# Kernel optimization log

Measured on AMD Instinct MI355X. Metric: run time of the kernel, lower is better.

Reference implementation:

```python
import jax, jax.numpy as jnp
import numpy as np
from jax import lax

WIN = 15      # sliding window size
BINS = 64     # luminance histogram bins
ALPHA = 0.9   # local vs global histogram mix
LAM1 = 0.5    # a-channel (material) removal weight
LAM2 = 0.5    # b-channel (material) removal weight
EPS = 1e-6


def _box_sum(x, win):
    return lax.reduce_window(x, 0.0, lax.add, (1, win, win, 1), (1, 1, 1, 1), 'SAME')


def setup_inputs() -> dict:
    key = jax.random.key(0)
    u = jax.random.uniform(key, (4, 3, 512, 512), dtype=jnp.float32)
    L = u[:, 0] * 100.0                 # L in [0,100]
    a = u[:, 1] * 255.0 - 128.0         # a in [-128,127]
    b = u[:, 2] * 255.0 - 128.0         # b in [-128,127]
    return {"batch_lab_raw": jnp.stack([L, a, b], axis=1)}


def reference(batch_lab_raw):
    # Normalize channels
    Ln = jnp.clip(batch_lab_raw[:, 0] / 100.0, 0.0, 1.0)      # (B,H,W)
    an = (batch_lab_raw[:, 1] + 128.0) / 255.0                # (B,H,W)
    bn = (batch_lab_raw[:, 2] + 128.0) / 255.0                # (B,H,W)

    # --- windowed luminance histogram anomaly ---
    idx = jnp.clip((Ln * BINS).astype(jnp.int32), 0, BINS - 1)            # (B,H,W)
    onehot = jax.nn.one_hot(idx, BINS, dtype=Ln.dtype)                    # (B,H,W,K)
    cnt = _box_sum(onehot, WIN)                                           # (B,H,W,K)
    n = _box_sum(jnp.ones(Ln.shape + (1,), Ln.dtype), WIN)                # (B,H,W,1) valid-pixel count
    # probability of own bin within local window
    p_loc = jnp.take_along_axis(cnt / n, idx[..., None], axis=-1)[..., 0]  # (B,H,W)
    # global per-image histogram probability of own bin
    p_glob_bins = jnp.mean(onehot, axis=(1, 2))                            # (B,K)
    p_glob = jnp.einsum('bhwk,bk->bhw', onehot, p_glob_bins)              # (B,H,W)

    S = -jnp.log(ALPHA * p_loc + (1.0 - ALPHA) * p_glob + EPS)            # surprise
    S_min = jnp.min(S, axis=(1, 2), keepdims=True)
    S_max = jnp.max(S, axis=(1, 2), keepdims=True)
    L_anom_norm = (S - S_min) / (S_max - S_min + EPS)                     # (B,H,W)

    # --- de-materialized illumination: remove local chroma (material) variation ---
    mu_a = _box_sum(an[..., None], WIN)[..., 0] / n[..., 0]
    mu_b = _box_sum(bn[..., None], WIN)[..., 0] / n[..., 0]
    L_perp = jnp.clip(Ln - LAM1 * (an - mu_a) - LAM2 * (bn - mu_b), 0.0, 1.0)

    return (L_perp[:, None], L_anom_norm[:, None])  # each (B,1,H,W)
```

## Files before the change

### kernel.cpp

```cpp
#include <hip/hip_runtime.h>

#define Hh 512
#define Ww 512
#define NPIX (Hh*Ww)
#define BATCH 4


__global__ __launch_bounds__(256) void k_hist(const float* __restrict__ in,
                                              unsigned* __restrict__ hp) {
    __shared__ unsigned lh[64];
    const int tid = threadIdx.x;
    if (tid < 64) lh[tid] = 0u;
    __syncthreads();
    const int img = blockIdx.x >> 6, sub = blockIdx.x & 63;
    const float4* Lp = (const float4*)(in + (size_t)img * 3 * NPIX) + sub * 1024;
    #pragma unroll
    for (int t = 0; t < 4; ++t) {
        float4 v = Lp[t*256 + tid];
        float f[4] = {v.x, v.y, v.z, v.w};
        #pragma unroll
        for (int j = 0; j < 4; ++j) {
            float ln = fminf(fmaxf(f[j] / 100.0f, 0.0f), 1.0f);
            int idx = min((int)(ln * 64.0f), 63);
            atomicAdd(&lh[idx], 1u);
        }
    }
    __syncthreads();
    if (tid < 64) hp[(img*64 + sub)*64 + tid] = lh[tid];
}

__global__ __launch_bounds__(256, 8) void k_main(const float* __restrict__ in,
        const unsigned* __restrict__ hp, float* __restrict__ bmin,
        float* __restrict__ bmax, float* __restrict__ out)
{
    __shared__ unsigned s_pk[46*12];
    __shared__ float s_c[46*36];
    __shared__ float s_cc[32*33];
    __shared__ float s_lnc[32*16];
    __shared__ float lhf[64];
    __shared__ float red[8];

    const int tx = threadIdx.x, ty = threadIdx.y;
    const int tid = ty*16 + tx;
    const int bx = blockIdx.x * 16, by = blockIdx.y * 32;
    const int img = blockIdx.z;
    const float* Lp = in + (size_t)img * 3 * NPIX;

    if (tid < 64) {
        unsigned sum = 0;
        const unsigned* p = hp + img*4096 + tid;
        #pragma unroll 8
        for (int q = 0; q < 64; ++q) sum += p[q*64];
        lhf[tid] = (float)sum * (1.0f/262144.0f);
    }

    const int s = tx + 1;
    const int j0 = s >> 2;
    const unsigned m20 = 0x7FFFu << (s & 3);
    unsigned wm[5];
    #pragma unroll
    for (int i = 0; i < 5; ++i) {
        unsigned n = (m20 >> (4*i)) & 0xFu;
        wm[i] = (n&1u)*0x80u | (n&2u)*0x4000u | (n&4u)*0x200000u | (n&8u)*0x10000000u;
    }

    for (int l = tid; l < 368; l += 256) {
        const int r = l >> 3, c4 = l & 7;
        const int gy = by - 7 + r;
        const int gx0 = bx - 8 + c4*4;
        unsigned pk = 0x7F7F7F7Fu;
        float4 cv = {0.f, 0.f, 0.f, 0.f};
        if (gy >= 0 && gy < Hh && gx0 >= 0 && gx0 < Ww) {
            const int g = gy*Ww + gx0;
            const float4 Lv = *(const float4*)(Lp + g);
            const float4 Av = *(const float4*)(Lp + NPIX + g);
            const float4 Bv = *(const float4*)(Lp + 2*NPIX + g);
            const float l0 = fminf(fmaxf(Lv.x / 100.0f, 0.0f), 1.0f);
            const float l1 = fminf(fmaxf(Lv.y / 100.0f, 0.0f), 1.0f);
            const float l2 = fminf(fmaxf(Lv.z / 100.0f, 0.0f), 1.0f);
            const float l3 = fminf(fmaxf(Lv.w / 100.0f, 0.0f), 1.0f);
            const int b0 = min((int)(l0*64.0f), 63), b1 = min((int)(l1*64.0f), 63);
            const int b2 = min((int)(l2*64.0f), 63), b3 = min((int)(l3*64.0f), 63);
            pk = (unsigned)b0 | ((unsigned)b1<<8) | ((unsigned)b2<<16) | ((unsigned)b3<<24);
            const float k255 = 1.0f/255.0f;
            cv.x = (Av.x+128.0f)*k255 + (Bv.x+128.0f)*k255;
            cv.y = (Av.y+128.0f)*k255 + (Bv.y+128.0f)*k255;
            cv.z = (Av.z+128.0f)*k255 + (Bv.z+128.0f)*k255;
            cv.w = (Av.w+128.0f)*k255 + (Bv.w+128.0f)*k255;
            if (r >= 7 && r < 39 && c4 >= 2 && c4 <= 5) {
                float4 lv4 = {l0, l1, l2, l3};
                *(float4*)&s_lnc[(r-7)*16 + 4*(c4-2)] = lv4;
            }
        }
        s_pk[r*12 + c4] = pk;
        *(float4*)&s_c[r*36 + c4*4] = cv;
    }
    for (int l = tid; l < 184; l += 256) s_pk[(l>>2)*12 + 8 + (l&3)] = 0u;
    __syncthreads();

    for (int l = tid; l < 512; l += 256) {
        const int q = l >> 5, c = l & 31;
        float mid = 0.f;
        #pragma unroll
        for (int k = 1; k < 15; ++k) mid += s_c[(2*q+k)*36 + c];
        s_cc[(2*q)*33 + c]   = mid + s_c[(2*q)*36 + c];
        s_cc[(2*q+1)*33 + c] = mid + s_c[(2*q+15)*36 + c];
    }
    __syncthreads();

    const int r0 = 2*ty;
    const int cbyte = tx + 8;
    const unsigned cb0 = (s_pk[(r0+7)*12 + (cbyte>>2)] >> (8*(cbyte&3))) & 0xFFu;
    const unsigned cb1 = (s_pk[(r0+8)*12 + (cbyte>>2)] >> (8*(cbyte&3))) & 0xFFu;
    const unsigned cb40 = cb0 * 0x01010101u;
    const unsigned cb41 = cb1 * 0x01010101u;
    const unsigned K = 0x7F7F7F7Fu;
    int c0 = 0, c1 = 0;
    const unsigned* rp = s_pk + r0*12 + j0;

    {
        unsigned d0=rp[0], d1=rp[1], d2=rp[2], d3=rp[3], d4=rp[4];
        c0 += __popc(~((d0^cb40)+K) & wm[0]);
        c0 += __popc(~((d1^cb40)+K) & wm[1]);
        c0 += __popc(~((d2^cb40)+K) & wm[2]);
        c0 += __popc(~((d3^cb40)+K) & wm[3]);
        c0 += __popc(~((d4^cb40)+K) & wm[4]);
    }
    #pragma unroll 2
    for (int k = 1; k < 15; ++k) {
        const unsigned* rk = rp + k*12;
        unsigned d0=rk[0], d1=rk[1], d2=rk[2], d3=rk[3], d4=rk[4];
        c0 += __popc(~((d0^cb40)+K) & wm[0]);
        c1 += __popc(~((d0^cb41)+K) & wm[0]);
        c0 += __popc(~((d1^cb40)+K) & wm[1]);
        c1 += __popc(~((d1^cb41)+K) & wm[1]);
        c0 += __popc(~((d2^cb40)+K) & wm[2]);
        c1 += __popc(~((d2^cb41)+K) & wm[2]);
        c0 += __popc(~((d3^cb40)+K) & wm[3]);
        c1 += __popc(~((d3^cb41)+K) & wm[3]);
        c0 += __popc(~((d4^cb40)+K) & wm[4]);
        c1 += __popc(~((d4^cb41)+K) & wm[4]);
    }
    {
        const unsigned* rk = rp + 180;
        unsigned d0=rk[0], d1=rk[1], d2=rk[2], d3=rk[3], d4=rk[4];
        c1 += __popc(~((d0^cb41)+K) & wm[0]);
        c1 += __popc(~((d1^cb41)+K) & wm[1]);
        c1 += __popc(~((d2^cb41)+K) & wm[2]);
        c1 += __popc(~((d3^cb41)+K) & wm[3]);
        c1 += __popc(~((d4^cb41)+K) & wm[4]);
    }

    float sc0 = 0.f, sc1 = 0.f;
    const float* ccp = s_cc + r0*33 + s;
    #pragma unroll
    for (int dx = 0; dx < 15; ++dx) { sc0 += ccp[dx]; sc1 += ccp[33+dx]; }

    const int gx = bx + tx;
    const int gy0 = by + r0;
    const int cols  = min(gx+7, Ww-1) - max(gx-7, 0) + 1;
    const int rows0 = min(gy0+7, Hh-1) - max(gy0-7, 0) + 1;
    const int rows1 = min(gy0+8, Hh-1) - max(gy0-6, 0) + 1;
    const float inv0 = __builtin_amdgcn_rcpf((float)(rows0*cols));
    const float inv1 = __builtin_amdgcn_rcpf((float)(rows1*cols));
    const float pg0 = lhf[cb0];
    const float pg1 = lhf[cb1];
    const float S0 = -__logf(0.9f*((float)c0*inv0) + 0.1f*pg0 + 1e-6f);
    const float S1 = -__logf(0.9f*((float)c1*inv1) + 0.1f*pg1 + 1e-6f);
    const int gbase = img*NPIX + gy0*Ww + gx;

    const float lp0 = s_lnc[r0*16 + tx]     - 0.5f*(s_c[(r0+7)*36 + tx+8] - sc0*inv0);
    const float lp1 = s_lnc[(r0+1)*16 + tx] - 0.5f*(s_c[(r0+8)*36 + tx+8] - sc1*inv1);
    out[gbase]      = fminf(fmaxf(lp0, 0.f), 1.f);
    out[gbase + Ww] = fminf(fmaxf(lp1, 0.f), 1.f);
    float* outN = out + (size_t)BATCH*NPIX;
    outN[gbase]      = S0;
    outN[gbase + Ww] = S1;

    float smin = fminf(S0, S1), smax = fmaxf(S0, S1);
    #pragma unroll
    for (int off = 32; off >= 1; off >>= 1) {
        smin = fminf(smin, __shfl_xor(smin, off));
        smax = fmaxf(smax, __shfl_xor(smax, off));
    }
    const int wid = tid >> 6;
    if ((tid & 63) == 0) { red[wid] = smin; red[4+wid] = smax; }
    __syncthreads();
    if (tid == 0) {
        const int bid = blockIdx.y*32 + blockIdx.x;
        bmin[img*512 + bid] = fminf(fminf(red[0],red[1]), fminf(red[2],red[3]));
        bmax[img*512 + bid] = fmaxf(fmaxf(red[4],red[5]), fmaxf(red[6],red[7]));
    }
}

__global__ __launch_bounds__(256) void k_norm(float* __restrict__ outN,
        const float* __restrict__ bmin, const float* __restrict__ bmax) {
    __shared__ float red[8];
    const int tid = threadIdx.x;
    const int img = blockIdx.x >> 8;

    float mn = __builtin_inff(), mx = -__builtin_inff();
    if (tid < 128) {
        float4 a = ((const float4*)(bmin + img*512))[tid];
        float4 b = ((const float4*)(bmax + img*512))[tid];
        mn = fminf(fminf(a.x, a.y), fminf(a.z, a.w));
        mx = fmaxf(fmaxf(b.x, b.y), fmaxf(b.z, b.w));
    }
    #pragma unroll
    for (int off = 32; off >= 1; off >>= 1) {
        mn = fminf(mn, __shfl_xor(mn, off));
        mx = fmaxf(mx, __shfl_xor(mx, off));
    }
    if ((tid & 63) == 0) { red[tid>>6] = mn; red[4 + (tid>>6)] = mx; }
    __syncthreads();
    const float vmin = fminf(fminf(red[0],red[1]), fminf(red[2],red[3]));
    const float vmax = fmaxf(fmaxf(red[4],red[5]), fmaxf(red[6],red[7]));
    const float inv = 1.0f / (vmax - vmin + 1e-6f);

    float4* p = (float4*)outN + (size_t)blockIdx.x*256;
    float4 v = p[tid];
    v.x = (v.x - vmin) * inv; v.y = (v.y - vmin) * inv;
    v.z = (v.z - vmin) * inv; v.w = (v.w - vmin) * inv;
    p[tid] = v;
}

extern "C" void kernel_launch(void* const* d_in, const int* in_sizes, int n_in,
                              void* d_out, int out_size, void* d_ws, size_t ws_size,
                              hipStream_t stream) {
    const float* in = (const float*)d_in[0];
    float* out = (float*)d_out;
    float* bmin = (float*)d_ws;
    float* bmax = bmin + BATCH*512;
    unsigned* hp = (unsigned*)(bmax + BATCH*512);

    k_hist<<<BATCH*64, 256, 0, stream>>>(in, hp);
    dim3 grid(Ww/16, Hh/32, BATCH), blk(16, 16);
    k_main<<<grid, blk, 0, stream>>>(in, hp, bmin, bmax, out);
    k_norm<<<BATCH*256, 256, 0, stream>>>(out + (size_t)BATCH*NPIX, bmin, bmax);
}
```

Baseline: 84.85 us.

## Transpose partial-histogram layout, issue tile loads early, and compact packed-bin LDS rows

The histogram kernel now writes partial histograms bin-major, so the main kernel reduces each bin with four contiguous uint4 loads and two wave shuffles instead of 64 strided scalar loads. Tile loading first issues all global float4 loads for both iterations, then does the conversion, which raises memory-level parallelism. The packed-bin LDS row stride drops from 12 to 9 words and the zero-fill of padding columns is removed; column 8 of each row is left uninitialized and is read only under a zero mask. The popcount window loop is fully unrolled with four independent accumulators to shorten dependency chains, at some cost in code size and registers.

```diff
diff --git a/kernel.cpp b/kernel.cpp
--- a/kernel.cpp
+++ b/kernel.cpp
@@ -26,14 +26,14 @@
         }
     }
     __syncthreads();
-    if (tid < 64) hp[(img*64 + sub)*64 + tid] = lh[tid];
+    if (tid < 64) hp[((size_t)img*64 + tid)*64 + sub] = lh[tid];
 }
 
 __global__ __launch_bounds__(256, 8) void k_main(const float* __restrict__ in,
         const unsigned* __restrict__ hp, float* __restrict__ bmin,
         float* __restrict__ bmax, float* __restrict__ out)
 {
-    __shared__ unsigned s_pk[46*12];
+    __shared__ unsigned s_pk[46*9];
     __shared__ float s_c[46*36];
     __shared__ float s_cc[32*33];
     __shared__ float s_lnc[32*16];
@@ -46,12 +46,15 @@
     const int img = blockIdx.z;
     const float* Lp = in + (size_t)img * 3 * NPIX;
 
-    if (tid < 64) {
-        unsigned sum = 0;
-        const unsigned* p = hp + img*4096 + tid;
-        #pragma unroll 8
-        for (int q = 0; q < 64; ++q) sum += p[q*64];
-        lhf[tid] = (float)sum * (1.0f/262144.0f);
+    {
+        const int bin = tid >> 2, grp = tid & 3;
+        const uint4* p = (const uint4*)(hp + ((size_t)img*64 + bin)*64 + grp*16);
+        uint4 x0 = p[0], x1 = p[1], x2 = p[2], x3 = p[3];
+        unsigned sum = x0.x+x0.y+x0.z+x0.w + x1.x+x1.y+x1.z+x1.w
+                     + x2.x+x2.y+x2.z+x2.w + x3.x+x3.y+x3.z+x3.w;
+        sum += __shfl_xor(sum, 1);
+        sum += __shfl_xor(sum, 2);
+        if (grp == 0) lhf[bin] = (float)sum * (1.0f/262144.0f);
     }
 
     const int s = tx + 1;
@@ -64,38 +67,50 @@
         wm[i] = (n&1u)*0x80u | (n&2u)*0x4000u | (n&4u)*0x200000u | (n&8u)*0x10000000u;
     }
 
-    for (int l = tid; l < 368; l += 256) {
+    float4 Lv[2], Av[2], Bv[2];
+    bool vld[2];
+    #pragma unroll
+    for (int it = 0; it < 2; ++it) {
+        const int l = tid + it*256;
         const int r = l >> 3, c4 = l & 7;
-        const int gy = by - 7 + r;
-        const int gx0 = bx - 8 + c4*4;
-        unsigned pk = 0x7F7F7F7Fu;
-        float4 cv = {0.f, 0.f, 0.f, 0.f};
-        if (gy >= 0 && gy < Hh && gx0 >= 0 && gx0 < Ww) {
+        const int gy = by - 7 + r, gx0 = bx - 8 + c4*4;
+        vld[it] = (l < 368) && gy >= 0 && gy < Hh && gx0 >= 0 && gx0 < Ww;
+        if (vld[it]) {
             const int g = gy*Ww + gx0;
-            const float4 Lv = *(const float4*)(Lp + g);
-            const float4 Av = *(const float4*)(Lp + NPIX + g);
-            const float4 Bv = *(const float4*)(Lp + 2*NPIX + g);
-            const float l0 = fminf(fmaxf(Lv.x / 100.0f, 0.0f), 1.0f);
-            const float l1 = fminf(fmaxf(Lv.y / 100.0f, 0.0f), 1.0f);
-            const float l2 = fminf(fmaxf(Lv.z / 100.0f, 0.0f), 1.0f);
-            const float l3 = fminf(fmaxf(Lv.w / 100.0f, 0.0f), 1.0f);
-            const int b0 = min((int)(l0*64.0f), 63), b1 = min((int)(l1*64.0f), 63);
-            const int b2 = min((int)(l2*64.0f), 63), b3 = min((int)(l3*64.0f), 63);
-            pk = (unsigned)b0 | ((unsigned)b1<<8) | ((unsigned)b2<<16) | ((unsigned)b3<<24);
-            const float k255 = 1.0f/255.0f;
-            cv.x = (Av.x+128.0f)*k255 + (Bv.x+128.0f)*k255;
-            cv.y = (Av.y+128.0f)*k255 + (Bv.y+128.0f)*k255;
-            cv.z = (Av.z+128.0f)*k255 + (Bv.z+128.0f)*k255;
-            cv.w = (Av.w+128.0f)*k255 + (Bv.w+128.0f)*k255;
-            if (r >= 7 && r < 39 && c4 >= 2 && c4 <= 5) {
-                float4 lv4 = {l0, l1, l2, l3};
-                *(float4*)&s_lnc[(r-7)*16 + 4*(c4-2)] = lv4;
+            Lv[it] = *(const float4*)(Lp + g);
+            Av[it] = *(const float4*)(Lp + NPIX + g);
+            Bv[it] = *(const float4*)(Lp + 2*NPIX + g);
+        }
+    }
+    #pragma unroll
+    for (int it = 0; it < 2; ++it) {
+        const int l = tid + it*256;
+        if (l < 368) {
+            const int r = l >> 3, c4 = l & 7;
+            unsigned pk = 0x7F7F7F7Fu;
+            float4 cv = {0.f, 0.f, 0.f, 0.f};
+            if (vld[it]) {
+                const float l0 = fminf(fmaxf(Lv[it].x / 100.0f, 0.0f), 1.0f);
+                const float l1 = fminf(fmaxf(Lv[it].y / 100.0f, 0.0f), 1.0f);
+                const float l2 = fminf(fmaxf(Lv[it].z / 100.0f, 0.0f), 1.0f);
+                const float l3 = fminf(fmaxf(Lv[it].w / 100.0f, 0.0f), 1.0f);
+                const int b0 = min((int)(l0*64.0f), 63), b1 = min((int)(l1*64.0f), 63);
+                const int b2 = min((int)(l2*64.0f), 63), b3 = min((int)(l3*64.0f), 63);
+                pk = (unsigned)b0 | ((unsigned)b1<<8) | ((unsigned)b2<<16) | ((unsigned)b3<<24);
+                const float k255 = 1.0f/255.0f;
+                cv.x = (Av[it].x+128.0f)*k255 + (Bv[it].x+128.0f)*k255;
+                cv.y = (Av[it].y+128.0f)*k255 + (Bv[it].y+128.0f)*k255;
+                cv.z = (Av[it].z+128.0f)*k255 + (Bv[it].z+128.0f)*k255;
+                cv.w = (Av[it].w+128.0f)*k255 + (Bv[it].w+128.0f)*k255;
+                if (r >= 7 && r < 39 && c4 >= 2 && c4 <= 5) {
+                    float4 lv4 = {l0, l1, l2, l3};
+                    *(float4*)&s_lnc[(r-7)*16 + 4*(c4-2)] = lv4;
+                }
             }
-        }
-        s_pk[r*12 + c4] = pk;
-        *(float4*)&s_c[r*36 + c4*4] = cv;
-    }
-    for (int l = tid; l < 184; l += 256) s_pk[(l>>2)*12 + 8 + (l&3)] = 0u;
+            s_pk[r*9 + c4] = pk;
+            *(float4*)&s_c[r*36 + c4*4] = cv;
+        }
+    }
     __syncthreads();
 
     for (int l = tid; l < 512; l += 256) {
@@ -110,46 +125,34 @@
 
     const int r0 = 2*ty;
     const int cbyte = tx + 8;
-    const unsigned cb0 = (s_pk[(r0+7)*12 + (cbyte>>2)] >> (8*(cbyte&3))) & 0xFFu;
-    const unsigned cb1 = (s_pk[(r0+8)*12 + (cbyte>>2)] >> (8*(cbyte&3))) & 0xFFu;
+    const unsigned cb0 = (s_pk[(r0+7)*9 + (cbyte>>2)] >> (8*(cbyte&3))) & 0xFFu;
+    const unsigned cb1 = (s_pk[(r0+8)*9 + (cbyte>>2)] >> (8*(cbyte&3))) & 0xFFu;
     const unsigned cb40 = cb0 * 0x01010101u;
     const unsigned cb41 = cb1 * 0x01010101u;
     const unsigned K = 0x7F7F7F7Fu;
-    int c0 = 0, c1 = 0;
-    const unsigned* rp = s_pk + r0*12 + j0;
-
-    {
-        unsigned d0=rp[0], d1=rp[1], d2=rp[2], d3=rp[3], d4=rp[4];
-        c0 += __popc(~((d0^cb40)+K) & wm[0]);
-        c0 += __popc(~((d1^cb40)+K) & wm[1]);
-        c0 += __popc(~((d2^cb40)+K) & wm[2]);
-        c0 += __popc(~((d3^cb40)+K) & wm[3]);
-        c0 += __popc(~((d4^cb40)+K) & wm[4]);
-    }
-    #pragma unroll 2
-    for (int k = 1; k < 15; ++k) {
-        const unsigned* rk = rp + k*12;
-        unsigned d0=rk[0], d1=rk[1], d2=rk[2], d3=rk[3], d4=rk[4];
-        c0 += __popc(~((d0^cb40)+K) & wm[0]);
-        c1 += __popc(~((d0^cb41)+K) & wm[0]);
-        c0 += __popc(~((d1^cb40)+K) & wm[1]);
-        c1 += __popc(~((d1^cb41)+K) & wm[1]);
-        c0 += __popc(~((d2^cb40)+K) & wm[2]);
-        c1 += __popc(~((d2^cb41)+K) & wm[2]);
-        c0 += __popc(~((d3^cb40)+K) & wm[3]);
-        c1 += __popc(~((d3^cb41)+K) & wm[3]);
-        c0 += __popc(~((d4^cb40)+K) & wm[4]);
-        c1 += __popc(~((d4^cb41)+K) & wm[4]);
-    }
-    {
-        const unsigned* rk = rp + 180;
-        unsigned d0=rk[0], d1=rk[1], d2=rk[2], d3=rk[3], d4=rk[4];
-        c1 += __popc(~((d0^cb41)+K) & wm[0]);
-        c1 += __popc(~((d1^cb41)+K) & wm[1]);
-        c1 += __popc(~((d2^cb41)+K) & wm[2]);
-        c1 += __popc(~((d3^cb41)+K) & wm[3]);
-        c1 += __popc(~((d4^cb41)+K) & wm[4]);
-    }
+    int a0 = 0, a1 = 0, a2 = 0, a3 = 0;
+    const unsigned* rp = s_pk + r0*9 + j0;
+
+    #pragma unroll
+    for (int k = 0; k < 16; ++k) {
+        const unsigned d0 = rp[k*9+0], d1 = rp[k*9+1], d2 = rp[k*9+2],
+                       d3 = rp[k*9+3], d4 = rp[k*9+4];
+        if (k != 15) {
+            a0 += __popc(~((d0^cb40)+K) & wm[0]);
+            a1 += __popc(~((d1^cb40)+K) & wm[1]);
+            a0 += __popc(~((d2^cb40)+K) & wm[2]);
+            a1 += __popc(~((d3^cb40)+K) & wm[3]);
+            a0 += __popc(~((d4^cb40)+K) & wm[4]);
+        }
+        if (k != 0) {
+            a2 += __popc(~((d0^cb41)+K) & wm[0]);
+            a3 += __popc(~((d1^cb41)+K) & wm[1]);
+            a2 += __popc(~((d2^cb41)+K) & wm[2]);
+            a3 += __popc(~((d3^cb41)+K) & wm[3]);
+            a2 += __popc(~((d4^cb41)+K) & wm[4]);
+        }
+    }
+    const int c0 = a0 + a1, c1 = a2 + a3;
 
     float sc0 = 0.f, sc1 = 0.f;
     const float* ccp = s_cc + r0*33 + s;
```

Result: no change. 83.94 us (-1.1%).
